# Performance work log

Measured on AMD Instinct MI355X. Metric: run time of the kernel, lower is better.

Reference implementation:

```python
import jax, jax.numpy as jnp
import numpy as np

T, B, H = 2048, 16, 1024


def setup_inputs() -> dict:
    key = jax.random.key(0)
    k1, k2, k3 = jax.random.split(key, 3)
    inputs = jax.random.normal(k1, (T, B, H), dtype=jnp.float32)
    # torch params initialized uniform_(-0.1, 0.1)
    weight_W = jax.random.uniform(k2, (H, H), dtype=jnp.float32, minval=-0.1, maxval=0.1)
    weight_proj = jax.random.uniform(k3, (H, 1), dtype=jnp.float32, minval=-0.1, maxval=0.1)
    return {"inputs": inputs, "weight_W": weight_W, "weight_proj": weight_proj,
            "attention_width": 3}


def reference(inputs, weight_W, weight_proj, attention_width):
    # inputs: [T, B, H] (time-major). For t < w the input passes through unchanged.
    # For t >= w: attend over the previous w steps (t-w .. t-1, excluding t):
    #   score_j = tanh(h_j @ W) @ proj, a = softmax over window, out = sum_j a_j * h_j
    w = attention_width
    t = inputs.shape[0]
    n = t - w  # number of attended output positions
    # per-position scores, computed once for all timesteps: [T, B]
    scores = jnp.squeeze(jnp.tanh(inputs @ weight_W) @ weight_proj, axis=-1)
    # sliding windows via w shifted views (w is small and static)
    s_win = jnp.stack([scores[j:j + n] for j in range(w)], axis=0)   # [w, n, B]
    v_win = jnp.stack([inputs[j:j + n] for j in range(w)], axis=0)   # [w, n, B, H]
    attn = jax.nn.softmax(s_win, axis=0)                             # softmax over window
    tail = jnp.einsum('wnb,wnbh->nbh', attn, v_win)                  # [n, B, H]
    return jnp.concatenate([inputs[:w], tail], axis=0)               # [T, B, H]
```

## Files before the change

kernel.cpp:

```cpp
#include <hip/hip_runtime.h>
#include <stdint.h>

#define T_DIM 2048
#define B_DIM 16
#define H_DIM 1024
#define M_DIM (T_DIM * B_DIM)
#define BK 64
#define TCHUNK 32

typedef __attribute__((ext_vector_type(8))) short bf16x8;
typedef __attribute__((ext_vector_type(4))) float floatx4;

__device__ inline unsigned short f2bf(float f) {
  union { float f; unsigned int u; } c; c.f = f;
  unsigned int u = c.u;
  return (unsigned short)((u + 0x7FFFu + ((u >> 16) & 1u)) >> 16);
}

__device__ inline float bf2f(unsigned short u) {
  union { float f; unsigned int u; } c; c.u = ((unsigned int)u) << 16;
  return c.f;
}

__device__ inline float fast_tanh(float x) {
  float e = __expf(2.0f * x);
  return 1.0f - 2.0f / (e + 1.0f);
}

__global__ void convert_x_kernel(const float* __restrict__ x,
                                 unsigned short* __restrict__ xb) {
  size_t i = ((size_t)blockIdx.x * 256 + threadIdx.x) * 4;
  float4 v = *(const float4*)(x + i);
  ushort4 o;
  o.x = f2bf(v.x); o.y = f2bf(v.y); o.z = f2bf(v.z); o.w = f2bf(v.w);
  *(ushort4*)(xb + i) = o;
}

__global__ void transpose_w_kernel(const float* __restrict__ w,
                                   unsigned short* __restrict__ wt) {
  __shared__ float tile[32][33];
  int tx = threadIdx.x, ty = threadIdx.y;
  int n0 = blockIdx.x * 32, k0 = blockIdx.y * 32;
  for (int i = ty; i < 32; i += 8)
    tile[i][tx] = w[(size_t)(k0 + i) * H_DIM + n0 + tx];
  __syncthreads();
  for (int i = ty; i < 32; i += 8)
    wt[(size_t)(n0 + i) * H_DIM + k0 + tx] = f2bf(tile[tx][i]);
}

__global__ __launch_bounds__(256, 4)
void score_gemm_kernel(const unsigned short* __restrict__ Xb,
                       const unsigned short* __restrict__ Wt,
                       const float* __restrict__ proj,
                       float* __restrict__ scores) {
  __shared__ __align__(16) unsigned short ldsA[128 * BK];
  __shared__ __align__(16) unsigned short ldsB[128 * BK];

  const int tid  = threadIdx.x;
  const int lane = tid & 63;
  const int wave = tid >> 6;
  const int wy = wave >> 1, wx = wave & 1;
  const int quad = lane >> 4, l16 = lane & 15;

  const int idx   = blockIdx.x;
  const int x7    = idx & 7;
  const int split = (idx >> 3) & 3;
  const int g     = idx >> 5;
  const int bm    = g * 8 + x7;
  const int m0    = bm * 128;
  const int nbase = split * 256;

  int ldsOff[4];
  int rowOff[4];
  #pragma unroll
  for (int i = 0; i < 4; ++i) {
    int cb = (i * 4 + wave) * 64;
    int s = cb + lane;
    int row = s >> 3, cs = s & 7;
    int cg = cs ^ (row & 7);
    ldsOff[i] = cb;
    rowOff[i] = row * H_DIM + cg * 8;
  }

  float sc[4][4];
  #pragma unroll
  for (int a = 0; a < 4; ++a)
    #pragma unroll
    for (int b = 0; b < 4; ++b) sc[a][b] = 0.0f;

  for (int n0 = nbase; n0 < nbase + 256; n0 += 128) {
    floatx4 acc[4][4];
    #pragma unroll
    for (int a = 0; a < 4; ++a)
      #pragma unroll
      for (int b = 0; b < 4; ++b) acc[a][b] = (floatx4){0.f, 0.f, 0.f, 0.f};

    for (int k0 = 0; k0 < H_DIM; k0 += BK) {
      #pragma unroll
      for (int i = 0; i < 4; ++i) {
        const unsigned short* ga = Xb + (size_t)m0 * H_DIM + rowOff[i] + k0;
        __builtin_amdgcn_global_load_lds(
            (const __attribute__((address_space(1))) void*)ga,
            (__attribute__((address_space(3))) void*)(&ldsA[ldsOff[i] * 8]),
            16, 0, 0);
        const unsigned short* gb = Wt + (size_t)n0 * H_DIM + rowOff[i] + k0;
        __builtin_amdgcn_global_load_lds(
            (const __attribute__((address_space(1))) void*)gb,
            (__attribute__((address_space(3))) void*)(&ldsB[ldsOff[i] * 8]),
            16, 0, 0);
      }
      __syncthreads();

      #pragma unroll
      for (int kk = 0; kk < BK; kk += 32) {
        const int c = (kk >> 3) + quad;
        bf16x8 af[4], bfr[4];
        #pragma unroll
        for (int rs = 0; rs < 4; ++rs) {
          int r = wy * 64 + rs * 16 + l16;
          af[rs] = *(const bf16x8*)&ldsA[(r * 8 + (c ^ (r & 7))) * 8];
        }
        #pragma unroll
        for (int ns = 0; ns < 4; ++ns) {
          int n = wx * 64 + ns * 16 + l16;
          bfr[ns] = *(const bf16x8*)&ldsB[(n * 8 + (c ^ (n & 7))) * 8];
        }
        #pragma unroll
        for (int rs = 0; rs < 4; ++rs)
          #pragma unroll
          for (int ns = 0; ns < 4; ++ns)
            acc[rs][ns] = __builtin_amdgcn_mfma_f32_16x16x32_bf16(
                af[rs], bfr[ns], acc[rs][ns], 0, 0, 0);
      }
      __syncthreads();
    }

    #pragma unroll
    for (int ns = 0; ns < 4; ++ns) {
      int n = n0 + wx * 64 + ns * 16 + l16;
      float p = proj[n];
      #pragma unroll
      for (int rs = 0; rs < 4; ++rs)
        #pragma unroll
        for (int gg = 0; gg < 4; ++gg)
          sc[rs][gg] += fast_tanh(acc[rs][ns][gg]) * p;
    }
  }

  #pragma unroll
  for (int rs = 0; rs < 4; ++rs)
    #pragma unroll
    for (int gg = 0; gg < 4; ++gg) {
      float v = sc[rs][gg];
      v += __shfl_xor(v, 1);
      v += __shfl_xor(v, 2);
      v += __shfl_xor(v, 4);
      v += __shfl_xor(v, 8);
      if (l16 == 0) {
        int row = m0 + wy * 64 + rs * 16 + quad * 4 + gg;
        atomicAdd(&scores[row], v);
      }
    }
}

__global__ void out_kernel_bf16(const float* __restrict__ x,
                                const unsigned short* __restrict__ xb,
                                const float* __restrict__ scores,
                                const int* __restrict__ wp,
                                float* __restrict__ out) {
  int w = *wp;
  int t0 = blockIdx.x * TCHUNK;
  int b  = blockIdx.y;
  int h  = threadIdx.x;
  const float4* x4 = (const float4*)x;
  float4* o4 = (float4*)out;
  const ushort4* xb4 = (const ushort4*)xb;

  if (w == 3) {
    float4 z = {0.f, 0.f, 0.f, 0.f};
    float4 a0, a1, a2;
    float  s0, s1, s2;
    #pragma unroll
    for (int j = 0; j < 3; ++j) {
      int tm = t0 - 3 + j;
      float4 a = z; float s = 0.f;
      if (tm >= 0) {
        ushort4 u = xb4[((size_t)tm * B_DIM + b) * 256 + h];
        a.x = bf2f(u.x); a.y = bf2f(u.y); a.z = bf2f(u.z); a.w = bf2f(u.w);
        s = scores[tm * B_DIM + b];
      }
      if (j == 0) { a0 = a; s0 = s; }
      else if (j == 1) { a1 = a; s1 = s; }
      else { a2 = a; s2 = s; }
    }
    for (int i = 0; i < TCHUNK; ++i) {
      int t = t0 + i;
      size_t rbase = ((size_t)t * B_DIM + b) * 256 + h;
      ushort4 u = xb4[rbase];
      float4 v;
      v.x = bf2f(u.x); v.y = bf2f(u.y); v.z = bf2f(u.z); v.w = bf2f(u.w);
      float sv = scores[t * B_DIM + b];
      if (t < 3) {
        o4[rbase] = x4[rbase];
      } else {
        float m = fmaxf(fmaxf(s0, s1), s2);
        float e0 = __expf(s0 - m), e1 = __expf(s1 - m), e2 = __expf(s2 - m);
        float inv = 1.0f / (e0 + e1 + e2);
        e0 *= inv; e1 *= inv; e2 *= inv;
        float4 o;
        o.x = e0 * a0.x + e1 * a1.x + e2 * a2.x;
        o.y = e0 * a0.y + e1 * a1.y + e2 * a2.y;
        o.z = e0 * a0.z + e1 * a1.z + e2 * a2.z;
        o.w = e0 * a0.w + e1 * a1.w + e2 * a2.w;
        o4[rbase] = o;
      }
      a0 = a1; a1 = a2; a2 = v;
      s0 = s1; s1 = s2; s2 = sv;
    }
  } else {
    if (w > 8) w = 8;
    for (int i = 0; i < TCHUNK; ++i) {
      int t = t0 + i;
      size_t rbase = ((size_t)t * B_DIM + b) * 256 + h;
      if (t < w) { o4[rbase] = x4[rbase]; continue; }
      float s[8];
      float mx = -1e30f;
      for (int j = 0; j < w; ++j) {
        s[j] = scores[(t - w + j) * B_DIM + b];
        mx = fmaxf(mx, s[j]);
      }
      float sum = 0.f;
      for (int j = 0; j < w; ++j) { s[j] = __expf(s[j] - mx); sum += s[j]; }
      float inv = 1.0f / sum;
      float4 o = {0.f, 0.f, 0.f, 0.f};
      for (int j = 0; j < w; ++j) {
        float a = s[j] * inv;
        float4 v = x4[((size_t)(t - w + j) * B_DIM + b) * 256 + h];
        o.x += a * v.x; o.y += a * v.y; o.z += a * v.z; o.w += a * v.w;
      }
      o4[rbase] = o;
    }
  }
}

__global__ void out_kernel_f32(const float* __restrict__ x,
                               const float* __restrict__ scores,
                               const int* __restrict__ wp,
                               float* __restrict__ out) {
  int w = *wp;
  int t0 = blockIdx.x * TCHUNK;
  int b  = blockIdx.y;
  int h  = threadIdx.x;
  const float4* x4 = (const float4*)x;
  float4* o4 = (float4*)out;

  if (w == 3) {
    float4 z = {0.f, 0.f, 0.f, 0.f};
    float4 a0, a1, a2;
    float  s0, s1, s2;
    {
      int tm = t0 - 3;
      a0 = (tm >= 0) ? x4[((size_t)tm * B_DIM + b) * 256 + h] : z;
      s0 = (tm >= 0) ? scores[tm * B_DIM + b] : 0.f;
      tm = t0 - 2;
      a1 = (tm >= 0) ? x4[((size_t)tm * B_DIM + b) * 256 + h] : z;
      s1 = (tm >= 0) ? scores[tm * B_DIM + b] : 0.f;
      tm = t0 - 1;
      a2 = (tm >= 0) ? x4[((size_t)tm * B_DIM + b) * 256 + h] : z;
      s2 = (tm >= 0) ? scores[tm * B_DIM + b] : 0.f;
    }
    for (int i = 0; i < TCHUNK; ++i) {
      int t = t0 + i;
      size_t rbase = ((size_t)t * B_DIM + b) * 256 + h;
      float4 v = x4[rbase];
      float  sv = scores[t * B_DIM + b];
      if (t < 3) {
        o4[rbase] = v;
      } else {
        float m = fmaxf(fmaxf(s0, s1), s2);
        float e0 = __expf(s0 - m), e1 = __expf(s1 - m), e2 = __expf(s2 - m);
        float inv = 1.0f / (e0 + e1 + e2);
        e0 *= inv; e1 *= inv; e2 *= inv;
        float4 o;
        o.x = e0 * a0.x + e1 * a1.x + e2 * a2.x;
        o.y = e0 * a0.y + e1 * a1.y + e2 * a2.y;
        o.z = e0 * a0.z + e1 * a1.z + e2 * a2.z;
        o.w = e0 * a0.w + e1 * a1.w + e2 * a2.w;
        o4[rbase] = o;
      }
      a0 = a1; a1 = a2; a2 = v;
      s0 = s1; s1 = s2; s2 = sv;
    }
  } else {
    if (w > 8) w = 8;
    for (int i = 0; i < TCHUNK; ++i) {
      int t = t0 + i;
      size_t rbase = ((size_t)t * B_DIM + b) * 256 + h;
      if (t < w) { o4[rbase] = x4[rbase]; continue; }
      float s[8];
      float mx = -1e30f;
      for (int j = 0; j < w; ++j) {
        s[j] = scores[(t - w + j) * B_DIM + b];
        mx = fmaxf(mx, s[j]);
      }
      float sum = 0.f;
      for (int j = 0; j < w; ++j) { s[j] = __expf(s[j] - mx); sum += s[j]; }
      float inv = 1.0f / sum;
      float4 o = {0.f, 0.f, 0.f, 0.f};
      for (int j = 0; j < w; ++j) {
        float a = s[j] * inv;
        float4 v = x4[((size_t)(t - w + j) * B_DIM + b) * 256 + h];
        o.x += a * v.x; o.y += a * v.y; o.z += a * v.z; o.w += a * v.w;
      }
      o4[rbase] = o;
    }
  }
}

extern "C" void kernel_launch(void* const* d_in, const int* in_sizes, int n_in,
                              void* d_out, int out_size, void* d_ws, size_t ws_size,
                              hipStream_t stream) {
  const float* x    = (const float*)d_in[0];
  const float* w    = (const float*)d_in[1];
  const float* proj = (const float*)d_in[2];
  const int*   wp   = (const int*)d_in[3];
  float* out = (float*)d_out;

  const size_t XB_BYTES = (size_t)64 * 1024 * 1024;
  const size_t WT_BYTES = (size_t)2 * 1024 * 1024;
  const size_t need = XB_BYTES + WT_BYTES + (size_t)M_DIM * sizeof(float);
  const bool use_ws = ws_size >= need;

  unsigned short* Xb;
  unsigned short* Wt;
  float* scores;
  if (use_ws) {
    Xb = (unsigned short*)d_ws;
    Wt = (unsigned short*)((char*)d_ws + XB_BYTES);
    scores = (float*)((char*)d_ws + XB_BYTES + WT_BYTES);
  } else {
    Xb = (unsigned short*)d_out;
    Wt = (unsigned short*)((char*)d_out + XB_BYTES);
    scores = (float*)d_ws;
  }

  hipMemsetAsync(scores, 0, M_DIM * sizeof(float), stream);

  convert_x_kernel<<<M_DIM * H_DIM / 1024, 256, 0, stream>>>(x, Xb);
  transpose_w_kernel<<<dim3(32, 32), dim3(32, 8), 0, stream>>>(w, Wt);
  score_gemm_kernel<<<1024, 256, 0, stream>>>(Xb, Wt, proj, scores);
  if (use_ws)
    out_kernel_bf16<<<dim3(T_DIM / TCHUNK, B_DIM), 256, 0, stream>>>(x, Xb, scores, wp, out);
  else
    out_kernel_f32<<<dim3(T_DIM / TCHUNK, B_DIM), 256, 0, stream>>>(x, scores, wp, out);
}
```

Baseline: 335.2 us.

## Rewrite score GEMM as 256x256-tile, 8-wave, double-buffered pipelined MFMA kernel

Restructures the score GEMM from 128x128 tiles with 4 waves and synchronous K-steps into 256x256 tiles with 8 waves. It double-buffers LDS and issues async global-to-LDS loads for later K-slices, interleaved between MFMA phases with explicit barriers, vmcnt waits and setprio. The goal is to hide global load latency, raise MFMA utilisation and halve redundant A/B traffic through bigger tiles. In exchange it uses 128KB of LDS and more accumulator registers, which limits occupancy, and the hand-coded waitcnt and barrier schedule is fragile.

```diff
diff --git a/kernel.cpp b/kernel.cpp
--- a/kernel.cpp
+++ b/kernel.cpp
@@ -5,11 +5,17 @@
 #define B_DIM 16
 #define H_DIM 1024
 #define M_DIM (T_DIM * B_DIM)
-#define BK 64
 #define TCHUNK 32
 
 typedef __attribute__((ext_vector_type(8))) short bf16x8;
 typedef __attribute__((ext_vector_type(4))) float floatx4;
+
+#define BARRIER() asm volatile("s_barrier" ::: "memory")
+#define LGKM0()                                            \
+  do {                                                     \
+    asm volatile("s_waitcnt lgkmcnt(0)" ::: "memory");     \
+    __builtin_amdgcn_sched_barrier(0);                     \
+  } while (0)
 
 __device__ inline unsigned short f2bf(float f) {
   union { float f; unsigned int u; } c; c.f = f;
@@ -25,6 +31,13 @@
 __device__ inline float fast_tanh(float x) {
   float e = __expf(2.0f * x);
   return 1.0f - 2.0f / (e + 1.0f);
+}
+
+__device__ __forceinline__ void glds16(const unsigned short* g,
+                                       const unsigned short* l) {
+  __builtin_amdgcn_global_load_lds(
+      (const __attribute__((address_space(1))) void*)g,
+      (__attribute__((address_space(3))) void*)l, 16, 0, 0);
 }
 
 __global__ void convert_x_kernel(const float* __restrict__ x,
@@ -48,18 +61,19 @@
     wt[(size_t)(n0 + i) * H_DIM + k0 + tx] = f2bf(tile[tx][i]);
 }
 
-__global__ __launch_bounds__(256, 4)
+__global__ __launch_bounds__(512, 2)
 void score_gemm_kernel(const unsigned short* __restrict__ Xb,
                        const unsigned short* __restrict__ Wt,
                        const float* __restrict__ proj,
                        float* __restrict__ scores) {
-  __shared__ __align__(16) unsigned short ldsA[128 * BK];
-  __shared__ __align__(16) unsigned short ldsB[128 * BK];
+  __shared__ __align__(16) unsigned short ldsA[32768];
+  __shared__ __align__(16) unsigned short ldsB[32768];
 
   const int tid  = threadIdx.x;
   const int lane = tid & 63;
   const int wave = tid >> 6;
-  const int wy = wave >> 1, wx = wave & 1;
+  const int wy   = wave >> 2;
+  const int wx   = wave & 3;
   const int quad = lane >> 4, l16 = lane & 15;
 
   const int idx   = blockIdx.x;
@@ -67,97 +81,172 @@
   const int split = (idx >> 3) & 3;
   const int g     = idx >> 5;
   const int bm    = g * 8 + x7;
-  const int m0    = bm * 128;
-  const int nbase = split * 256;
-
-  int ldsOff[4];
-  int rowOff[4];
+  const int m0    = bm * 256;
+  const int n0    = split * 256;
+
+  int gOff0, gOff1, lB0, lB1;
+  {
+    int ci0 = wave * 64 + lane;
+    int r0  = ci0 >> 3;
+    gOff0 = r0 * H_DIM + (((ci0 & 7) ^ (r0 & 7)) * 8);
+    lB0   = (wave * 64) * 8;
+    int ci1 = ci0 + 512;
+    int r1  = ci1 >> 3;
+    gOff1 = r1 * H_DIM + (((ci1 & 7) ^ (r1 & 7)) * 8);
+    lB1   = (wave * 64 + 512) * 8;
+  }
+
+  const int cg0 = quad ^ (l16 & 7);
+  const int cg1 = (quad + 4) ^ (l16 & 7);
+
+  auto issue_ht = [&](int h) {
+    int th = h >> 2, ht = h & 3;
+    int base = (th & 1) * 16384 + (ht & 1) * 8192;
+    int k0 = th * 64;
+    if (ht & 2) {
+      const unsigned short* gs =
+          Xb + (size_t)(m0 + (ht & 1) * 128) * H_DIM + k0;
+      glds16(gs + gOff0, &ldsA[base + lB0]);
+      glds16(gs + gOff1, &ldsA[base + lB1]);
+    } else {
+      const unsigned short* gs =
+          Wt + (size_t)(n0 + (ht & 1) * 128) * H_DIM + k0;
+      glds16(gs + gOff0, &ldsB[base + lB0]);
+      glds16(gs + gOff1, &ldsB[base + lB1]);
+    }
+  };
+
+  floatx4 acc[8][4];
   #pragma unroll
-  for (int i = 0; i < 4; ++i) {
-    int cb = (i * 4 + wave) * 64;
-    int s = cb + lane;
-    int row = s >> 3, cs = s & 7;
-    int cg = cs ^ (row & 7);
-    ldsOff[i] = cb;
-    rowOff[i] = row * H_DIM + cg * 8;
-  }
-
-  float sc[4][4];
+  for (int m = 0; m < 8; ++m)
+    #pragma unroll
+    for (int n = 0; n < 4; ++n) acc[m][n] = (floatx4){0.f, 0.f, 0.f, 0.f};
+
   #pragma unroll
-  for (int a = 0; a < 4; ++a)
-    #pragma unroll
-    for (int b = 0; b < 4; ++b) sc[a][b] = 0.0f;
-
-  for (int n0 = nbase; n0 < nbase + 256; n0 += 128) {
-    floatx4 acc[4][4];
-    #pragma unroll
-    for (int a = 0; a < 4; ++a)
-      #pragma unroll
-      for (int b = 0; b < 4; ++b) acc[a][b] = (floatx4){0.f, 0.f, 0.f, 0.f};
-
-    for (int k0 = 0; k0 < H_DIM; k0 += BK) {
-      #pragma unroll
-      for (int i = 0; i < 4; ++i) {
-        const unsigned short* ga = Xb + (size_t)m0 * H_DIM + rowOff[i] + k0;
-        __builtin_amdgcn_global_load_lds(
-            (const __attribute__((address_space(1))) void*)ga,
-            (__attribute__((address_space(3))) void*)(&ldsA[ldsOff[i] * 8]),
-            16, 0, 0);
-        const unsigned short* gb = Wt + (size_t)n0 * H_DIM + rowOff[i] + k0;
-        __builtin_amdgcn_global_load_lds(
-            (const __attribute__((address_space(1))) void*)gb,
-            (__attribute__((address_space(3))) void*)(&ldsB[ldsOff[i] * 8]),
-            16, 0, 0);
-      }
-      __syncthreads();
-
-      #pragma unroll
-      for (int kk = 0; kk < BK; kk += 32) {
-        const int c = (kk >> 3) + quad;
-        bf16x8 af[4], bfr[4];
-        #pragma unroll
-        for (int rs = 0; rs < 4; ++rs) {
-          int r = wy * 64 + rs * 16 + l16;
-          af[rs] = *(const bf16x8*)&ldsA[(r * 8 + (c ^ (r & 7))) * 8];
-        }
-        #pragma unroll
-        for (int ns = 0; ns < 4; ++ns) {
-          int n = wx * 64 + ns * 16 + l16;
-          bfr[ns] = *(const bf16x8*)&ldsB[(n * 8 + (c ^ (n & 7))) * 8];
-        }
-        #pragma unroll
-        for (int rs = 0; rs < 4; ++rs)
-          #pragma unroll
-          for (int ns = 0; ns < 4; ++ns)
-            acc[rs][ns] = __builtin_amdgcn_mfma_f32_16x16x32_bf16(
-                af[rs], bfr[ns], acc[rs][ns], 0, 0, 0);
-      }
-      __syncthreads();
-    }
-
-    #pragma unroll
-    for (int ns = 0; ns < 4; ++ns) {
-      int n = n0 + wx * 64 + ns * 16 + l16;
-      float p = proj[n];
+  for (int h = 0; h < 6; ++h) issue_ht(h);
+  asm volatile("s_waitcnt vmcnt(4)" ::: "memory");
+  BARRIER();
+
+  int cur = 0;
+  for (int t = 0; t < 16; ++t) {
+    const int aB = cur * 16384 + wy * 8192;
+    const int bB = cur * 16384 + (wx >> 1) * 8192;
+    const int nL = (wx & 1) * 64;
+
+    bf16x8 af[4][2], bfr[2][2][2];
+
+    #pragma unroll
+    for (int rs = 0; rs < 4; ++rs) {
+      int r = rs * 16 + l16;
+      af[rs][0] = *(const bf16x8*)&ldsA[aB + r * 64 + cg0 * 8];
+      af[rs][1] = *(const bf16x8*)&ldsA[aB + r * 64 + cg1 * 8];
+    }
+    #pragma unroll
+    for (int ns = 0; ns < 2; ++ns) {
+      int n = nL + ns * 16 + l16;
+      bfr[0][ns][0] = *(const bf16x8*)&ldsB[bB + n * 64 + cg0 * 8];
+      bfr[0][ns][1] = *(const bf16x8*)&ldsB[bB + n * 64 + cg1 * 8];
+    }
+    { int h = 4 * t + 6; if (h < 64) issue_ht(h); }
+    BARRIER();
+    LGKM0();
+    __builtin_amdgcn_s_setprio(1);
+    #pragma unroll
+    for (int k = 0; k < 2; ++k)
       #pragma unroll
       for (int rs = 0; rs < 4; ++rs)
         #pragma unroll
-        for (int gg = 0; gg < 4; ++gg)
-          sc[rs][gg] += fast_tanh(acc[rs][ns][gg]) * p;
-    }
+        for (int ns = 0; ns < 2; ++ns)
+          acc[rs][ns] = __builtin_amdgcn_mfma_f32_16x16x32_bf16(
+              af[rs][k], bfr[0][ns][k], acc[rs][ns], 0, 0, 0);
+    __builtin_amdgcn_s_setprio(0);
+    BARRIER();
+
+    #pragma unroll
+    for (int ns = 0; ns < 2; ++ns) {
+      int n = nL + 32 + ns * 16 + l16;
+      bfr[1][ns][0] = *(const bf16x8*)&ldsB[bB + n * 64 + cg0 * 8];
+      bfr[1][ns][1] = *(const bf16x8*)&ldsB[bB + n * 64 + cg1 * 8];
+    }
+    { int h = 4 * t + 7; if (h < 64) issue_ht(h); }
+    BARRIER();
+    LGKM0();
+    __builtin_amdgcn_s_setprio(1);
+    #pragma unroll
+    for (int k = 0; k < 2; ++k)
+      #pragma unroll
+      for (int rs = 0; rs < 4; ++rs)
+        #pragma unroll
+        for (int ns = 0; ns < 2; ++ns)
+          acc[rs][2 + ns] = __builtin_amdgcn_mfma_f32_16x16x32_bf16(
+              af[rs][k], bfr[1][ns][k], acc[rs][2 + ns], 0, 0, 0);
+    __builtin_amdgcn_s_setprio(0);
+    BARRIER();
+
+    #pragma unroll
+    for (int rs = 0; rs < 4; ++rs) {
+      int r = 64 + rs * 16 + l16;
+      af[rs][0] = *(const bf16x8*)&ldsA[aB + r * 64 + cg0 * 8];
+      af[rs][1] = *(const bf16x8*)&ldsA[aB + r * 64 + cg1 * 8];
+    }
+    { int h = 4 * t + 8; if (h < 64) issue_ht(h); }
+    BARRIER();
+    LGKM0();
+    __builtin_amdgcn_s_setprio(1);
+    #pragma unroll
+    for (int k = 0; k < 2; ++k)
+      #pragma unroll
+      for (int rs = 0; rs < 4; ++rs)
+        #pragma unroll
+        for (int ns = 0; ns < 2; ++ns)
+          acc[4 + rs][2 + ns] = __builtin_amdgcn_mfma_f32_16x16x32_bf16(
+              af[rs][k], bfr[1][ns][k], acc[4 + rs][2 + ns], 0, 0, 0);
+    __builtin_amdgcn_s_setprio(0);
+    BARRIER();
+
+    { int h = 4 * t + 9; if (h < 64) issue_ht(h); }
+    BARRIER();
+    LGKM0();
+    __builtin_amdgcn_s_setprio(1);
+    #pragma unroll
+    for (int k = 0; k < 2; ++k)
+      #pragma unroll
+      for (int rs = 0; rs < 4; ++rs)
+        #pragma unroll
+        for (int ns = 0; ns < 2; ++ns)
+          acc[4 + rs][ns] = __builtin_amdgcn_mfma_f32_16x16x32_bf16(
+              af[rs][k], bfr[0][ns][k], acc[4 + rs][ns], 0, 0, 0);
+    __builtin_amdgcn_s_setprio(0);
+    if (t < 14) asm volatile("s_waitcnt vmcnt(4)" ::: "memory");
+    else        asm volatile("s_waitcnt vmcnt(0)" ::: "memory");
+    BARRIER();
+
+    cur ^= 1;
   }
 
+  float pv[2][2];
   #pragma unroll
-  for (int rs = 0; rs < 4; ++rs)
+  for (int nq = 0; nq < 2; ++nq)
+    #pragma unroll
+    for (int ns = 0; ns < 2; ++ns)
+      pv[nq][ns] = proj[n0 + wx * 64 + nq * 32 + ns * 16 + l16];
+
+  #pragma unroll
+  for (int m = 0; m < 8; ++m)
     #pragma unroll
     for (int gg = 0; gg < 4; ++gg) {
-      float v = sc[rs][gg];
+      float v = 0.f;
+      #pragma unroll
+      for (int nq = 0; nq < 2; ++nq)
+        #pragma unroll
+        for (int ns = 0; ns < 2; ++ns)
+          v += fast_tanh(acc[m][nq * 2 + ns][gg]) * pv[nq][ns];
       v += __shfl_xor(v, 1);
       v += __shfl_xor(v, 2);
       v += __shfl_xor(v, 4);
       v += __shfl_xor(v, 8);
       if (l16 == 0) {
-        int row = m0 + wy * 64 + rs * 16 + quad * 4 + gg;
+        int row = m0 + wy * 128 + (m >> 2) * 64 + (m & 3) * 16 + quad * 4 + gg;
         atomicAdd(&scores[row], v);
       }
     }
@@ -348,7 +437,7 @@
 
   convert_x_kernel<<<M_DIM * H_DIM / 1024, 256, 0, stream>>>(x, Xb);
   transpose_w_kernel<<<dim3(32, 32), dim3(32, 8), 0, stream>>>(w, Wt);
-  score_gemm_kernel<<<1024, 256, 0, stream>>>(Xb, Wt, proj, scores);
+  score_gemm_kernel<<<512, 512, 0, stream>>>(Xb, Wt, proj, scores);
   if (use_ws)
     out_kernel_bf16<<<dim3(T_DIM / TCHUNK, B_DIM), 256, 0, stream>>>(x, Xb, scores, wp, out);
   else
```

Result: slower. 343.7 us (+2.5%).

## Fuse fp32-to-bf16 conversion of X into GEMM loads and drop atomics

Applied to the files above, without the earlier changes.

The separate pass that converts X to bf16 is removed. The score GEMM now streams fp32 X straight into LDS, using a new swizzle, and converts it to bf16 in registers with v_cvt_pk_bf16_f32 before the MFMA. The atomicAdd reduction and its memset are replaced by 8 partial-score planes that the output kernel sums, and the output kernel reads fp32 X directly. This removes a 128MB read plus 64MB write pass and the atomics. In exchange, each K-tile moves twice the A bytes into LDS, LDS use rises so occupancy drops (launch bounds go from 4 to 3), and the output kernel does 8 reads per score.

```diff
diff --git a/kernel.cpp b/kernel.cpp
--- a/kernel.cpp
+++ b/kernel.cpp
@@ -17,23 +17,18 @@
   return (unsigned short)((u + 0x7FFFu + ((u >> 16) & 1u)) >> 16);
 }
 
-__device__ inline float bf2f(unsigned short u) {
-  union { float f; unsigned int u; } c; c.u = ((unsigned int)u) << 16;
-  return c.f;
-}
-
 __device__ inline float fast_tanh(float x) {
   float e = __expf(2.0f * x);
   return 1.0f - 2.0f / (e + 1.0f);
 }
 
-__global__ void convert_x_kernel(const float* __restrict__ x,
-                                 unsigned short* __restrict__ xb) {
-  size_t i = ((size_t)blockIdx.x * 256 + threadIdx.x) * 4;
-  float4 v = *(const float4*)(x + i);
-  ushort4 o;
-  o.x = f2bf(v.x); o.y = f2bf(v.y); o.z = f2bf(v.z); o.w = f2bf(v.w);
-  *(ushort4*)(xb + i) = o;
+__device__ __forceinline__ bf16x8 cvt8(float4 lo, float4 hi) {
+  union { bf16x8 v; unsigned int u[4]; } r;
+  asm("v_cvt_pk_bf16_f32 %0, %1, %2" : "=v"(r.u[0]) : "v"(lo.x), "v"(lo.y));
+  asm("v_cvt_pk_bf16_f32 %0, %1, %2" : "=v"(r.u[1]) : "v"(lo.z), "v"(lo.w));
+  asm("v_cvt_pk_bf16_f32 %0, %1, %2" : "=v"(r.u[2]) : "v"(hi.x), "v"(hi.y));
+  asm("v_cvt_pk_bf16_f32 %0, %1, %2" : "=v"(r.u[3]) : "v"(hi.z), "v"(hi.w));
+  return r.v;
 }
 
 __global__ void transpose_w_kernel(const float* __restrict__ w,
@@ -48,13 +43,13 @@
     wt[(size_t)(n0 + i) * H_DIM + k0 + tx] = f2bf(tile[tx][i]);
 }
 
-__global__ __launch_bounds__(256, 4)
-void score_gemm_kernel(const unsigned short* __restrict__ Xb,
+__global__ __launch_bounds__(256, 3)
+void score_gemm_kernel(const float* __restrict__ X,
                        const unsigned short* __restrict__ Wt,
                        const float* __restrict__ proj,
-                       float* __restrict__ scores) {
-  __shared__ __align__(16) unsigned short ldsA[128 * BK];
-  __shared__ __align__(16) unsigned short ldsB[128 * BK];
+                       float* __restrict__ scoresP) {
+  __shared__ __align__(16) float ldsAf[128 * 64];
+  __shared__ __align__(16) unsigned short ldsB[128 * 64];
 
   const int tid  = threadIdx.x;
   const int lane = tid & 63;
@@ -70,16 +65,24 @@
   const int m0    = bm * 128;
   const int nbase = split * 256;
 
-  int ldsOff[4];
-  int rowOff[4];
+  int gOffA[8], ldsAOff[8];
+  #pragma unroll
+  for (int i = 0; i < 8; ++i) {
+    int s = i * 256 + wave * 64 + lane;
+    int row = s >> 4, gg = s & 15;
+    int sg = gg ^ (row & 15);
+    gOffA[i] = row * H_DIM + sg * 4;
+    ldsAOff[i] = (i * 256 + wave * 64) * 4;
+  }
+  int gOffB[4], ldsBOff[4];
   #pragma unroll
   for (int i = 0; i < 4; ++i) {
     int cb = (i * 4 + wave) * 64;
     int s = cb + lane;
     int row = s >> 3, cs = s & 7;
     int cg = cs ^ (row & 7);
-    ldsOff[i] = cb;
-    rowOff[i] = row * H_DIM + cg * 8;
+    gOffB[i] = row * H_DIM + cg * 8;
+    ldsBOff[i] = cb * 8;
   }
 
   float sc[4][4];
@@ -97,16 +100,19 @@
 
     for (int k0 = 0; k0 < H_DIM; k0 += BK) {
       #pragma unroll
-      for (int i = 0; i < 4; ++i) {
-        const unsigned short* ga = Xb + (size_t)m0 * H_DIM + rowOff[i] + k0;
+      for (int i = 0; i < 8; ++i) {
+        const float* ga = X + (size_t)m0 * H_DIM + gOffA[i] + k0;
         __builtin_amdgcn_global_load_lds(
             (const __attribute__((address_space(1))) void*)ga,
-            (__attribute__((address_space(3))) void*)(&ldsA[ldsOff[i] * 8]),
+            (__attribute__((address_space(3))) void*)(&ldsAf[ldsAOff[i]]),
             16, 0, 0);
-        const unsigned short* gb = Wt + (size_t)n0 * H_DIM + rowOff[i] + k0;
+      }
+      #pragma unroll
+      for (int i = 0; i < 4; ++i) {
+        const unsigned short* gb = Wt + (size_t)n0 * H_DIM + gOffB[i] + k0;
         __builtin_amdgcn_global_load_lds(
             (const __attribute__((address_space(1))) void*)gb,
-            (__attribute__((address_space(3))) void*)(&ldsB[ldsOff[i] * 8]),
+            (__attribute__((address_space(3))) void*)(&ldsB[ldsBOff[i]]),
             16, 0, 0);
       }
       __syncthreads();
@@ -118,7 +124,11 @@
         #pragma unroll
         for (int rs = 0; rs < 4; ++rs) {
           int r = wy * 64 + rs * 16 + l16;
-          af[rs] = *(const bf16x8*)&ldsA[(r * 8 + (c ^ (r & 7))) * 8];
+          const float4 lo =
+              *(const float4*)&ldsAf[r * 64 + (((2 * c)     ^ (r & 15)) << 2)];
+          const float4 hi =
+              *(const float4*)&ldsAf[r * 64 + (((2 * c + 1) ^ (r & 15)) << 2)];
+          af[rs] = cvt8(lo, hi);
         }
         #pragma unroll
         for (int ns = 0; ns < 4; ++ns) {
@@ -158,101 +168,28 @@
       v += __shfl_xor(v, 8);
       if (l16 == 0) {
         int row = m0 + wy * 64 + rs * 16 + quad * 4 + gg;
-        atomicAdd(&scores[row], v);
-      }
-    }
-}
-
-__global__ void out_kernel_bf16(const float* __restrict__ x,
-                                const unsigned short* __restrict__ xb,
-                                const float* __restrict__ scores,
-                                const int* __restrict__ wp,
-                                float* __restrict__ out) {
+        scoresP[(size_t)(split * 2 + wx) * M_DIM + row] = v;
+      }
+    }
+}
+
+__global__ void out_kernel(const float* __restrict__ x,
+                           const float* __restrict__ sp,
+                           const int* __restrict__ wp,
+                           float* __restrict__ out) {
   int w = *wp;
   int t0 = blockIdx.x * TCHUNK;
   int b  = blockIdx.y;
   int h  = threadIdx.x;
   const float4* x4 = (const float4*)x;
   float4* o4 = (float4*)out;
-  const ushort4* xb4 = (const ushort4*)xb;
-
-  if (w == 3) {
-    float4 z = {0.f, 0.f, 0.f, 0.f};
-    float4 a0, a1, a2;
-    float  s0, s1, s2;
-    #pragma unroll
-    for (int j = 0; j < 3; ++j) {
-      int tm = t0 - 3 + j;
-      float4 a = z; float s = 0.f;
-      if (tm >= 0) {
-        ushort4 u = xb4[((size_t)tm * B_DIM + b) * 256 + h];
-        a.x = bf2f(u.x); a.y = bf2f(u.y); a.z = bf2f(u.z); a.w = bf2f(u.w);
-        s = scores[tm * B_DIM + b];
-      }
-      if (j == 0) { a0 = a; s0 = s; }
-      else if (j == 1) { a1 = a; s1 = s; }
-      else { a2 = a; s2 = s; }
-    }
-    for (int i = 0; i < TCHUNK; ++i) {
-      int t = t0 + i;
-      size_t rbase = ((size_t)t * B_DIM + b) * 256 + h;
-      ushort4 u = xb4[rbase];
-      float4 v;
-      v.x = bf2f(u.x); v.y = bf2f(u.y); v.z = bf2f(u.z); v.w = bf2f(u.w);
-      float sv = scores[t * B_DIM + b];
-      if (t < 3) {
-        o4[rbase] = x4[rbase];
-      } else {
-        float m = fmaxf(fmaxf(s0, s1), s2);
-        float e0 = __expf(s0 - m), e1 = __expf(s1 - m), e2 = __expf(s2 - m);
-        float inv = 1.0f / (e0 + e1 + e2);
-        e0 *= inv; e1 *= inv; e2 *= inv;
-        float4 o;
-        o.x = e0 * a0.x + e1 * a1.x + e2 * a2.x;
-        o.y = e0 * a0.y + e1 * a1.y + e2 * a2.y;
-        o.z = e0 * a0.z + e1 * a1.z + e2 * a2.z;
-        o.w = e0 * a0.w + e1 * a1.w + e2 * a2.w;
-        o4[rbase] = o;
-      }
-      a0 = a1; a1 = a2; a2 = v;
-      s0 = s1; s1 = s2; s2 = sv;
-    }
-  } else {
-    if (w > 8) w = 8;
-    for (int i = 0; i < TCHUNK; ++i) {
-      int t = t0 + i;
-      size_t rbase = ((size_t)t * B_DIM + b) * 256 + h;
-      if (t < w) { o4[rbase] = x4[rbase]; continue; }
-      float s[8];
-      float mx = -1e30f;
-      for (int j = 0; j < w; ++j) {
-        s[j] = scores[(t - w + j) * B_DIM + b];
-        mx = fmaxf(mx, s[j]);
-      }
-      float sum = 0.f;
-      for (int j = 0; j < w; ++j) { s[j] = __expf(s[j] - mx); sum += s[j]; }
-      float inv = 1.0f / sum;
-      float4 o = {0.f, 0.f, 0.f, 0.f};
-      for (int j = 0; j < w; ++j) {
-        float a = s[j] * inv;
-        float4 v = x4[((size_t)(t - w + j) * B_DIM + b) * 256 + h];
-        o.x += a * v.x; o.y += a * v.y; o.z += a * v.z; o.w += a * v.w;
-      }
-      o4[rbase] = o;
-    }
-  }
-}
-
-__global__ void out_kernel_f32(const float* __restrict__ x,
-                               const float* __restrict__ scores,
-                               const int* __restrict__ wp,
-                               float* __restrict__ out) {
-  int w = *wp;
-  int t0 = blockIdx.x * TCHUNK;
-  int b  = blockIdx.y;
-  int h  = threadIdx.x;
-  const float4* x4 = (const float4*)x;
-  float4* o4 = (float4*)out;
+
+  auto SC = [&](int i) {
+    float s = 0.f;
+    #pragma unroll
+    for (int p = 0; p < 8; ++p) s += sp[(size_t)p * M_DIM + i];
+    return s;
+  };
 
   if (w == 3) {
     float4 z = {0.f, 0.f, 0.f, 0.f};
@@ -261,19 +198,19 @@
     {
       int tm = t0 - 3;
       a0 = (tm >= 0) ? x4[((size_t)tm * B_DIM + b) * 256 + h] : z;
-      s0 = (tm >= 0) ? scores[tm * B_DIM + b] : 0.f;
+      s0 = (tm >= 0) ? SC(tm * B_DIM + b) : 0.f;
       tm = t0 - 2;
       a1 = (tm >= 0) ? x4[((size_t)tm * B_DIM + b) * 256 + h] : z;
-      s1 = (tm >= 0) ? scores[tm * B_DIM + b] : 0.f;
+      s1 = (tm >= 0) ? SC(tm * B_DIM + b) : 0.f;
       tm = t0 - 1;
       a2 = (tm >= 0) ? x4[((size_t)tm * B_DIM + b) * 256 + h] : z;
-      s2 = (tm >= 0) ? scores[tm * B_DIM + b] : 0.f;
+      s2 = (tm >= 0) ? SC(tm * B_DIM + b) : 0.f;
     }
     for (int i = 0; i < TCHUNK; ++i) {
       int t = t0 + i;
       size_t rbase = ((size_t)t * B_DIM + b) * 256 + h;
       float4 v = x4[rbase];
-      float  sv = scores[t * B_DIM + b];
+      float  sv = SC(t * B_DIM + b);
       if (t < 3) {
         o4[rbase] = v;
       } else {
@@ -300,7 +237,7 @@
       float s[8];
       float mx = -1e30f;
       for (int j = 0; j < w; ++j) {
-        s[j] = scores[(t - w + j) * B_DIM + b];
+        s[j] = SC((t - w + j) * B_DIM + b);
         mx = fmaxf(mx, s[j]);
       }
       float sum = 0.f;
@@ -326,31 +263,21 @@
   const int*   wp   = (const int*)d_in[3];
   float* out = (float*)d_out;
 
-  const size_t XB_BYTES = (size_t)64 * 1024 * 1024;
   const size_t WT_BYTES = (size_t)2 * 1024 * 1024;
-  const size_t need = XB_BYTES + WT_BYTES + (size_t)M_DIM * sizeof(float);
-  const bool use_ws = ws_size >= need;
-
-  unsigned short* Xb;
+  const size_t SP_BYTES = (size_t)8 * M_DIM * sizeof(float);
+  const bool use_ws = ws_size >= WT_BYTES + SP_BYTES;
+
   unsigned short* Wt;
-  float* scores;
+  float* scoresP;
   if (use_ws) {
-    Xb = (unsigned short*)d_ws;
-    Wt = (unsigned short*)((char*)d_ws + XB_BYTES);
-    scores = (float*)((char*)d_ws + XB_BYTES + WT_BYTES);
+    Wt = (unsigned short*)d_ws;
+    scoresP = (float*)((char*)d_ws + WT_BYTES);
   } else {
-    Xb = (unsigned short*)d_out;
-    Wt = (unsigned short*)((char*)d_out + XB_BYTES);
-    scores = (float*)d_ws;
-  }
-
-  hipMemsetAsync(scores, 0, M_DIM * sizeof(float), stream);
-
-  convert_x_kernel<<<M_DIM * H_DIM / 1024, 256, 0, stream>>>(x, Xb);
+    Wt = (unsigned short*)d_out;
+    scoresP = (float*)d_ws;
+  }
+
   transpose_w_kernel<<<dim3(32, 32), dim3(32, 8), 0, stream>>>(w, Wt);
-  score_gemm_kernel<<<1024, 256, 0, stream>>>(Xb, Wt, proj, scores);
-  if (use_ws)
-    out_kernel_bf16<<<dim3(T_DIM / TCHUNK, B_DIM), 256, 0, stream>>>(x, Xb, scores, wp, out);
-  else
-    out_kernel_f32<<<dim3(T_DIM / TCHUNK, B_DIM), 256, 0, stream>>>(x, scores, wp, out);
-}
+  score_gemm_kernel<<<1024, 256, 0, stream>>>(x, Wt, proj, scoresP);
+  out_kernel<<<dim3(T_DIM / TCHUNK, B_DIM), 256, 0, stream>>>(x, scoresP, wp, out);
+}
```

New measurement: 349.8 us. +4.4%, slower.
